# Kernel optimization log

Hardware: AMD Instinct MI355X
Metric: run time of the kernel (lower is better)

Reference implementation:

```python
import jax, jax.numpy as jnp
import numpy as np

N = 100000
E = 1600000
D_IN = 64
D_OUT = 64
H = 4


def setup_inputs() -> dict:
    key = jax.random.key(0)
    ks = jax.random.split(key, 8)
    x = jax.random.normal(ks[0], (N, D_IN), dtype=jnp.float32)
    edge_index = jax.random.randint(ks[1], (2, E), 0, N, dtype=jnp.int64)
    edge_attr = jax.random.normal(ks[2], (E, D_IN), dtype=jnp.float32)
    s = 1.0 / np.sqrt(D_IN)
    Wq = jax.random.uniform(ks[3], (D_IN, D_OUT), jnp.float32, -s, s)
    Wk = jax.random.uniform(ks[4], (D_IN, D_OUT), jnp.float32, -s, s)
    Wv = jax.random.uniform(ks[5], (D_IN, D_OUT), jnp.float32, -s, s)
    We = jax.random.uniform(ks[6], (D_IN, D_OUT), jnp.float32, -s, s)
    be = jax.random.uniform(ks[7], (D_OUT,), jnp.float32, -s, s)
    return {"x": x, "edge_index": edge_index, "edge_attr": edge_attr,
            "Wq": Wq, "Wk": Wk, "Wv": Wv, "We": We, "be": be}


def reference(x, edge_index, edge_attr, Wq, Wk, Wv, We, be):
    src = edge_index[0]  # segment ids for softmax + scatter (dest of message)
    nbr = edge_index[1]  # gathered node per edge
    C = D_OUT // H

    Z = edge_attr * x[nbr]                      # [E, D_IN]
    q = (x @ Wq).reshape(N, H, C)               # [N, H, C]
    k = (Z @ Wk).reshape(E, H, C)               # [E, H, C]
    v = (Z @ Wv).reshape(E, H, C)               # [E, H, C]

    # per-edge, per-head attention logits
    scores = jnp.einsum('ehc,ehc->eh', q[src], k) / jnp.sqrt(jnp.float32(C))  # [E, H]

    # segment softmax over edges grouped by src node
    m = jax.ops.segment_max(scores, src, num_segments=N)            # [N, H]
    m = jnp.where(jnp.isfinite(m), m, 0.0)
    e = jnp.exp(scores - m[src])                                    # [E, H]
    denom = jax.ops.segment_sum(e, src, num_segments=N)             # [N, H]
    att = e / (denom[src] + 1e-16)                                  # [E, H]

    # weighted scatter-sum aggregation per head
    out = jax.ops.segment_sum(att[:, :, None] * v, src, num_segments=N)  # [N, H, C]
    out = out.reshape(N, D_OUT)

    edge_out = Z @ We + be                                          # [E, D_OUT]
    return out, edge_out
```

## Files before the change

kernel.cpp:

```cpp
#include <hip/hip_runtime.h>

#define NN 100000
#define NE 1600000

__global__ __launch_bounds__(256) void node_prep(
    const float* __restrict__ x, const float* __restrict__ Wq,
    const float* __restrict__ Wk, float* __restrict__ g,
    float* __restrict__ denom, float* __restrict__ out_nodes)
{
  __shared__ float wqT[64 * 68];
  __shared__ float wk[64 * 68];
  __shared__ float xs[4][68];
  __shared__ float qs[4][68];

  const int tid = threadIdx.x;
  for (int idx = tid; idx < 4096; idx += 256) {
    const int i = idx >> 6, j = idx & 63;
    wqT[j * 68 + i] = Wq[idx];
    wk[i * 68 + j]  = Wk[idx];
  }
  __syncthreads();

  const int wave = tid >> 6, lane = tid & 63;
  for (int base = blockIdx.x * 4; base < NN; base += gridDim.x * 4) {
    const int n = base + wave;
    const bool valid = (n < NN);
    if (valid) xs[wave][lane] = x[n * 64 + lane];
    __syncthreads();

    float qv = 0.f;
    #pragma unroll
    for (int i = 0; i < 64; i += 4) {
      const float4 xv = *(const float4*)&xs[wave][i];
      const float4 wv = *(const float4*)&wqT[lane * 68 + i];
      qv += xv.x * wv.x + xv.y * wv.y + xv.z * wv.z + xv.w * wv.w;
    }
    qs[wave][lane] = qv;
    __syncthreads();

    if (valid) {
      #pragma unroll
      for (int h = 0; h < 4; h++) {
        float gv = 0.f;
        #pragma unroll
        for (int c = 0; c < 16; c += 4) {
          const float4 q4 = *(const float4*)&qs[wave][h * 16 + c];
          const float4 w4 = *(const float4*)&wk[lane * 68 + h * 16 + c];
          gv += q4.x * w4.x + q4.y * w4.y + q4.z * w4.z + q4.w * w4.w;
        }
        g[n * 256 + h * 64 + lane] = gv;
      }
      out_nodes[n * 64 + lane] = 0.f;
      if (lane < 4) denom[n * 4 + lane] = 0.f;
    }
    __syncthreads();
  }
}

__global__ __launch_bounds__(256) void edge_pass(
    const float* __restrict__ x, const int* __restrict__ ei,
    const float* __restrict__ ea, const float* __restrict__ Wv,
    const float* __restrict__ We, const float* __restrict__ be,
    const float* __restrict__ g, float* __restrict__ denom,
    float* __restrict__ out_nodes, float* __restrict__ edge_out)
{
  const int tid  = threadIdx.x;
  const int lane = tid & 63;
  const int wgid = blockIdx.x * 4 + (tid >> 6);
  const int nw   = gridDim.x * 4;

  float wcol[64], vcol[64];
  #pragma unroll
  for (int i = 0; i < 64; i++) {
    wcol[i] = We[i * 64 + lane];
    vcol[i] = Wv[i * 64 + lane];
  }
  const float bias = be[lane];

  for (int e = wgid; e < NE; e += nw) {
    const int s = ei[e];
    const int d = ei[NE + e];
    const float zv = ea[e * 64 + lane] * x[d * 64 + lane];

    float p0 = zv * g[s * 256 + lane];
    float p1 = zv * g[s * 256 + 64 + lane];
    float p2 = zv * g[s * 256 + 128 + lane];
    float p3 = zv * g[s * 256 + 192 + lane];
    #pragma unroll
    for (int off = 32; off > 0; off >>= 1) {
      p0 += __shfl_xor(p0, off);
      p1 += __shfl_xor(p1, off);
      p2 += __shfl_xor(p2, off);
      p3 += __shfl_xor(p3, off);
    }
    const float e0 = __expf(p0 * 0.25f);
    const float e1 = __expf(p1 * 0.25f);
    const float e2 = __expf(p2 * 0.25f);
    const float e3 = __expf(p3 * 0.25f);

    if (lane < 4) {
      const float ev = (lane == 0) ? e0 : (lane == 1) ? e1 : (lane == 2) ? e2 : e3;
      atomicAdd(&denom[s * 4 + lane], ev);
    }

    float ae0 = bias, ae1 = 0.f, ae2 = 0.f, ae3 = 0.f;
    float av0 = 0.f,  av1 = 0.f, av2 = 0.f, av3 = 0.f;
    #pragma unroll
    for (int i = 0; i < 64; i += 4) {
      const float z0 = __int_as_float(__builtin_amdgcn_readlane(__float_as_int(zv), i + 0));
      const float z1 = __int_as_float(__builtin_amdgcn_readlane(__float_as_int(zv), i + 1));
      const float z2 = __int_as_float(__builtin_amdgcn_readlane(__float_as_int(zv), i + 2));
      const float z3 = __int_as_float(__builtin_amdgcn_readlane(__float_as_int(zv), i + 3));
      ae0 += z0 * wcol[i + 0];  av0 += z0 * vcol[i + 0];
      ae1 += z1 * wcol[i + 1];  av1 += z1 * vcol[i + 1];
      ae2 += z2 * wcol[i + 2];  av2 += z2 * vcol[i + 2];
      ae3 += z3 * wcol[i + 3];  av3 += z3 * vcol[i + 3];
    }
    edge_out[e * 64 + lane] = (ae0 + ae1) + (ae2 + ae3);

    const float vj = (av0 + av1) + (av2 + av3);
    const float eh = (lane < 16) ? e0 : (lane < 32) ? e1 : (lane < 48) ? e2 : e3;
    atomicAdd(&out_nodes[s * 64 + lane], eh * vj);
  }
}

__global__ __launch_bounds__(256) void normalize_nodes(
    float* __restrict__ out_nodes, const float* __restrict__ denom)
{
  const int i = blockIdx.x * 256 + threadIdx.x;
  if (i < NN * 64) {
    const int n = i >> 6;
    const int h = (i >> 4) & 3;
    out_nodes[i] = out_nodes[i] / (denom[n * 4 + h] + 1e-16f);
  }
}

extern "C" void kernel_launch(void* const* d_in, const int* in_sizes, int n_in,
                              void* d_out, int out_size, void* d_ws, size_t ws_size,
                              hipStream_t stream) {
  const float* x  = (const float*)d_in[0];
  const int*   ei = (const int*)d_in[1];
  const float* ea = (const float*)d_in[2];
  const float* Wq = (const float*)d_in[3];
  const float* Wk = (const float*)d_in[4];
  const float* Wv = (const float*)d_in[5];
  const float* We = (const float*)d_in[6];
  const float* be = (const float*)d_in[7];

  float* out_nodes = (float*)d_out;
  float* edge_out  = out_nodes + (size_t)NN * 64;

  float* g     = (float*)d_ws;
  float* denom = g + (size_t)NN * 256;

  node_prep<<<1024, 256, 0, stream>>>(x, Wq, Wk, g, denom, out_nodes);
  edge_pass<<<2048, 256, 0, stream>>>(x, ei, ea, Wv, We, be, g, denom,
                                      out_nodes, edge_out);
  normalize_nodes<<<(NN * 64 + 255) / 256, 256, 0, stream>>>(out_nodes, denom);
}
```

Baseline: 1.641 ms.

## Prefetch next edges' gathers in edge pass and drop LDS from node prep

The edge loop now software-pipelines its gathers: edge indices are loaded two iterations ahead, and the next edge's edge_attr, x row and g row are loaded one iteration ahead, to hide random-gather latency. The per-head score reduction is merged into one shuffle chain after two shared steps, so a single exp per lane replaces four. node_prep keeps Wq and Wk in registers and broadcasts values with readlane, removing shared memory and barriers. normalize_nodes is vectorised to float4 with a reciprocal multiply, and launch bounds add a minimum-occupancy hint. The prefetching raises register pressure in a kernel that already holds 128 weight registers per lane, which can reduce occupancy.

```diff
diff --git a/kernel.cpp b/kernel.cpp
--- a/kernel.cpp
+++ b/kernel.cpp
@@ -3,70 +3,66 @@
 #define NN 100000
 #define NE 1600000
 
-__global__ __launch_bounds__(256) void node_prep(
+__device__ __forceinline__ float rl(float v, int l) {
+  return __int_as_float(__builtin_amdgcn_readlane(__float_as_int(v), l));
+}
+
+__global__ __launch_bounds__(256, 2) void node_prep(
     const float* __restrict__ x, const float* __restrict__ Wq,
     const float* __restrict__ Wk, float* __restrict__ g,
     float* __restrict__ denom, float* __restrict__ out_nodes)
 {
-  __shared__ float wqT[64 * 68];
-  __shared__ float wk[64 * 68];
-  __shared__ float xs[4][68];
-  __shared__ float qs[4][68];
+  const int lane = threadIdx.x & 63;
+  const int wid  = __builtin_amdgcn_readfirstlane(blockIdx.x * 4 + (int)(threadIdx.x >> 6));
+  const int nw   = gridDim.x * 4;
 
-  const int tid = threadIdx.x;
-  for (int idx = tid; idx < 4096; idx += 256) {
-    const int i = idx >> 6, j = idx & 63;
-    wqT[j * 68 + i] = Wq[idx];
-    wk[i * 68 + j]  = Wk[idx];
+  float wq[64], wk[64];
+  #pragma unroll
+  for (int i = 0; i < 64; i++) {
+    wq[i] = Wq[i * 64 + lane];
+    wk[i] = Wk[lane * 64 + i];
   }
-  __syncthreads();
 
-  const int wave = tid >> 6, lane = tid & 63;
-  for (int base = blockIdx.x * 4; base < NN; base += gridDim.x * 4) {
-    const int n = base + wave;
-    const bool valid = (n < NN);
-    if (valid) xs[wave][lane] = x[n * 64 + lane];
-    __syncthreads();
+  for (int n = wid; n < NN; n += nw) {
+    const float xv = x[n * 64 + lane];
 
-    float qv = 0.f;
+    float q0 = 0.f, q1 = 0.f, q2 = 0.f, q3 = 0.f;
     #pragma unroll
     for (int i = 0; i < 64; i += 4) {
-      const float4 xv = *(const float4*)&xs[wave][i];
-      const float4 wv = *(const float4*)&wqT[lane * 68 + i];
-      qv += xv.x * wv.x + xv.y * wv.y + xv.z * wv.z + xv.w * wv.w;
+      q0 += rl(xv, i + 0) * wq[i + 0];
+      q1 += rl(xv, i + 1) * wq[i + 1];
+      q2 += rl(xv, i + 2) * wq[i + 2];
+      q3 += rl(xv, i + 3) * wq[i + 3];
     }
-    qs[wave][lane] = qv;
-    __syncthreads();
+    const float qv = (q0 + q1) + (q2 + q3);
 
-    if (valid) {
+    #pragma unroll
+    for (int h = 0; h < 4; h++) {
+      float g0 = 0.f, g1 = 0.f, g2 = 0.f, g3 = 0.f;
       #pragma unroll
-      for (int h = 0; h < 4; h++) {
-        float gv = 0.f;
-        #pragma unroll
-        for (int c = 0; c < 16; c += 4) {
-          const float4 q4 = *(const float4*)&qs[wave][h * 16 + c];
-          const float4 w4 = *(const float4*)&wk[lane * 68 + h * 16 + c];
-          gv += q4.x * w4.x + q4.y * w4.y + q4.z * w4.z + q4.w * w4.w;
-        }
-        g[n * 256 + h * 64 + lane] = gv;
+      for (int c = 0; c < 16; c += 4) {
+        g0 += rl(qv, h * 16 + c + 0) * wk[h * 16 + c + 0];
+        g1 += rl(qv, h * 16 + c + 1) * wk[h * 16 + c + 1];
+        g2 += rl(qv, h * 16 + c + 2) * wk[h * 16 + c + 2];
+        g3 += rl(qv, h * 16 + c + 3) * wk[h * 16 + c + 3];
       }
-      out_nodes[n * 64 + lane] = 0.f;
-      if (lane < 4) denom[n * 4 + lane] = 0.f;
+      g[n * 256 + h * 64 + lane] = (g0 + g1) + (g2 + g3);
     }
-    __syncthreads();
+
+    out_nodes[n * 64 + lane] = 0.f;
+    if (lane < 4) denom[n * 4 + lane] = 0.f;
   }
 }
 
-__global__ __launch_bounds__(256) void edge_pass(
+__global__ __launch_bounds__(256, 2) void edge_pass(
     const float* __restrict__ x, const int* __restrict__ ei,
     const float* __restrict__ ea, const float* __restrict__ Wv,
     const float* __restrict__ We, const float* __restrict__ be,
     const float* __restrict__ g, float* __restrict__ denom,
     float* __restrict__ out_nodes, float* __restrict__ edge_out)
 {
-  const int tid  = threadIdx.x;
-  const int lane = tid & 63;
-  const int wgid = blockIdx.x * 4 + (tid >> 6);
+  const int lane = threadIdx.x & 63;
+  const int wid  = __builtin_amdgcn_readfirstlane(blockIdx.x * 4 + (int)(threadIdx.x >> 6));
   const int nw   = gridDim.x * 4;
 
   float wcol[64], vcol[64];
@@ -77,61 +73,77 @@
   }
   const float bias = be[lane];
 
-  for (int e = wgid; e < NE; e += nw) {
-    const int s = ei[e];
-    const int d = ei[NE + e];
-    const float zv = ea[e * 64 + lane] * x[d * 64 + lane];
+  if (wid >= NE) return;
 
-    float p0 = zv * g[s * 256 + lane];
-    float p1 = zv * g[s * 256 + 64 + lane];
-    float p2 = zv * g[s * 256 + 128 + lane];
-    float p3 = zv * g[s * 256 + 192 + lane];
-    #pragma unroll
-    for (int off = 32; off > 0; off >>= 1) {
-      p0 += __shfl_xor(p0, off);
-      p1 += __shfl_xor(p1, off);
-      p2 += __shfl_xor(p2, off);
-      p3 += __shfl_xor(p3, off);
-    }
-    const float e0 = __expf(p0 * 0.25f);
-    const float e1 = __expf(p1 * 0.25f);
-    const float e2 = __expf(p2 * 0.25f);
-    const float e3 = __expf(p3 * 0.25f);
+  int e1 = (wid + nw < NE) ? wid + nw : wid;
+  int s0 = ei[wid], d0 = ei[NE + wid];
+  int s1 = ei[e1],  d1 = ei[NE + e1];
 
-    if (lane < 4) {
-      const float ev = (lane == 0) ? e0 : (lane == 1) ? e1 : (lane == 2) ? e2 : e3;
-      atomicAdd(&denom[s * 4 + lane], ev);
-    }
+  float eav = ea[(size_t)wid * 64 + lane];
+  float xvv = x [(size_t)d0  * 64 + lane];
+  const float* gp = g + (size_t)s0 * 256;
+  float g0 = gp[lane], g1 = gp[64 + lane], g2 = gp[128 + lane], g3 = gp[192 + lane];
+
+  for (int e = wid; e < NE; e += nw) {
+    const int e2 = (e + 2 * nw < NE) ? e + 2 * nw : e;
+    const int s2 = ei[e2], d2 = ei[NE + e2];
+
+    const float ean = ea[(size_t)e1 * 64 + lane];
+    const float xan = x [(size_t)d1 * 64 + lane];
+    const float* gn = g + (size_t)s1 * 256;
+    const float g0n = gn[lane], g1n = gn[64 + lane], g2n = gn[128 + lane], g3n = gn[192 + lane];
+
+    const float zv = eav * xvv;
+
+    float p0 = zv * g0, p1 = zv * g1, p2 = zv * g2, p3 = zv * g3;
+    p0 += __shfl_xor(p0, 32); p1 += __shfl_xor(p1, 32);
+    p2 += __shfl_xor(p2, 32); p3 += __shfl_xor(p3, 32);
+    p0 += __shfl_xor(p0, 16); p1 += __shfl_xor(p1, 16);
+    p2 += __shfl_xor(p2, 16); p3 += __shfl_xor(p3, 16);
+    float ph = (lane < 32) ? ((lane < 16) ? p0 : p1) : ((lane < 48) ? p2 : p3);
+    ph += __shfl_xor(ph, 8);
+    ph += __shfl_xor(ph, 4);
+    ph += __shfl_xor(ph, 2);
+    ph += __shfl_xor(ph, 1);
+    const float ev = __expf(ph * 0.25f);
+
+    if ((lane & 15) == 0) atomicAdd(&denom[s0 * 4 + (lane >> 4)], ev);
 
     float ae0 = bias, ae1 = 0.f, ae2 = 0.f, ae3 = 0.f;
     float av0 = 0.f,  av1 = 0.f, av2 = 0.f, av3 = 0.f;
     #pragma unroll
     for (int i = 0; i < 64; i += 4) {
-      const float z0 = __int_as_float(__builtin_amdgcn_readlane(__float_as_int(zv), i + 0));
-      const float z1 = __int_as_float(__builtin_amdgcn_readlane(__float_as_int(zv), i + 1));
-      const float z2 = __int_as_float(__builtin_amdgcn_readlane(__float_as_int(zv), i + 2));
-      const float z3 = __int_as_float(__builtin_amdgcn_readlane(__float_as_int(zv), i + 3));
+      const float z0 = rl(zv, i + 0);
+      const float z1 = rl(zv, i + 1);
+      const float z2 = rl(zv, i + 2);
+      const float z3 = rl(zv, i + 3);
       ae0 += z0 * wcol[i + 0];  av0 += z0 * vcol[i + 0];
       ae1 += z1 * wcol[i + 1];  av1 += z1 * vcol[i + 1];
       ae2 += z2 * wcol[i + 2];  av2 += z2 * vcol[i + 2];
       ae3 += z3 * wcol[i + 3];  av3 += z3 * vcol[i + 3];
     }
-    edge_out[e * 64 + lane] = (ae0 + ae1) + (ae2 + ae3);
+    edge_out[(size_t)e * 64 + lane] = (ae0 + ae1) + (ae2 + ae3);
 
     const float vj = (av0 + av1) + (av2 + av3);
-    const float eh = (lane < 16) ? e0 : (lane < 32) ? e1 : (lane < 48) ? e2 : e3;
-    atomicAdd(&out_nodes[s * 64 + lane], eh * vj);
+    atomicAdd(&out_nodes[s0 * 64 + lane], ev * vj);
+
+    s0 = s1; d0 = d1; s1 = s2; d1 = d2; e1 = e2;
+    eav = ean; xvv = xan;
+    g0 = g0n; g1 = g1n; g2 = g2n; g3 = g3n;
   }
 }
 
 __global__ __launch_bounds__(256) void normalize_nodes(
-    float* __restrict__ out_nodes, const float* __restrict__ denom)
+    float4* __restrict__ out4, const float* __restrict__ denom)
 {
   const int i = blockIdx.x * 256 + threadIdx.x;
-  if (i < NN * 64) {
-    const int n = i >> 6;
-    const int h = (i >> 4) & 3;
-    out_nodes[i] = out_nodes[i] / (denom[n * 4 + h] + 1e-16f);
+  if (i < NN * 16) {
+    const int n = i >> 4;
+    const int h = (i >> 2) & 3;
+    const float dv = 1.0f / (denom[n * 4 + h] + 1e-16f);
+    float4 v = out4[i];
+    v.x *= dv; v.y *= dv; v.z *= dv; v.w *= dv;
+    out4[i] = v;
   }
 }
 
@@ -156,5 +168,6 @@
   node_prep<<<1024, 256, 0, stream>>>(x, Wq, Wk, g, denom, out_nodes);
   edge_pass<<<2048, 256, 0, stream>>>(x, ei, ea, Wv, We, be, g, denom,
                                       out_nodes, edge_out);
-  normalize_nodes<<<(NN * 64 + 255) / 256, 256, 0, stream>>>(out_nodes, denom);
+  normalize_nodes<<<(NN * 16 + 255) / 256, 256, 0, stream>>>(
+      (float4*)out_nodes, denom);
 }
```

Result: faster. 1.532 ms (-6.7%).
